# Kernel optimization log

Measured on AMD Instinct MI355X. Metric: run time of the kernel, lower is better.

Reference implementation:

```python
import jax, jax.numpy as jnp
import numpy as np

LN_EPS = 1e-5
NRM_EPS = 1e-12


def layernorm(x, w, b):
    mu = x.mean(-1, keepdims=True)
    var = ((x - mu) ** 2).mean(-1, keepdims=True)
    return (x - mu) * jax.lax.rsqrt(var + LN_EPS) * w + b


def cdist(x, y):
    # Euclidean pairwise distance over trailing (N, C): (..., N, C) x (..., M, C) -> (..., N, M)
    x2 = (x * x).sum(-1)
    y2 = (y * y).sum(-1)
    xy = jnp.einsum('...ic,...jc->...ij', x, y)
    return jnp.sqrt(jnp.maximum(x2[..., :, None] + y2[..., None, :] - 2.0 * xy, NRM_EPS))


def l2norm_last(x):
    n = jnp.sqrt((x * x).sum(-1, keepdims=True))
    return x / jnp.maximum(n, NRM_EPS)


def attn_qcs_sd(anchor, positive, neg1, neg2, k, alpha):
    # anchor/positive: (B,N,C); neg1/neg2: (2,B,N,C)
    # torch.tensor(neg) in the original detaches neg1/neg2 from autograd
    neg1 = jax.lax.stop_gradient(neg1)
    neg2 = jax.lax.stop_gradient(neg2)
    k = k + 1.0
    S_p = cdist(positive, anchor)           # (B,N,N)
    S_p = S_p - S_p.min()
    S_p = S_p.max() - S_p
    S_a = l2norm_last(S_p).sum(1)           # (B,N)
    S_p1 = l2norm_last(jnp.swapaxes(S_p, 1, 2)).sum(1)  # (B,N)

    def proc(D):  # (B,N,N) -> (B,N)
        D = D - D.min()
        return l2norm_last(D).sum(1)

    def pair(neg, tgt):  # neg (2,B,N,C), tgt (B,N,C)
        D = cdist(neg, jnp.broadcast_to(tgt[None], neg.shape))  # (2,B,N,N)
        return proc(D[0]), proc(D[1])

    d11, d12 = pair(neg1, anchor)
    d21, d22 = pair(neg2, anchor)
    map1 = S_a + k * ((d11 + d12) / 2 * alpha + (1 - alpha) * ((d21 + d22) / 2))
    d11, d12 = pair(neg1, positive)
    d21, d22 = pair(neg2, positive)
    map2 = S_p1 + k * ((d11 + d12) / 2 * alpha + (1 - alpha) * ((d21 + d22) / 2))
    return map1[..., None], map2[..., None]  # (B,N,1) each


def setup_inputs() -> dict:
    key = jax.random.key(0)
    B, N, C = 8, 1024, 768
    ks = jax.random.split(key, 12)
    s = 1.0 / np.sqrt(C)
    sh = 1.0 / np.sqrt(4 * C)
    return {
        'anchor': jax.random.normal(ks[0], (B, N, C), jnp.float32),
        'positive': jax.random.normal(ks[1], (B, N, C), jnp.float32),
        'neg1': jax.random.normal(ks[2], (2, B, N, C), jnp.float32),
        'neg2': jax.random.normal(ks[3], (2, B, N, C), jnp.float32),
        'norm1_w': jnp.ones((C,), jnp.float32),
        'norm1_b': jnp.zeros((C,), jnp.float32),
        'norm2_w': jnp.ones((C,), jnp.float32),
        'norm2_b': jnp.zeros((C,), jnp.float32),
        'proj_W': jax.random.uniform(ks[4], (C, 2 * C), jnp.float32, -s, s),
        'proj_b': jax.random.uniform(ks[5], (2 * C,), jnp.float32, -s, s),
        'fc1_W': jax.random.uniform(ks[6], (C, 4 * C), jnp.float32, -s, s),
        'fc1_b': jax.random.uniform(ks[7], (4 * C,), jnp.float32, -s, s),
        'fc2_W': jax.random.uniform(ks[8], (4 * C, C), jnp.float32, -sh, sh),
        'fc2_b': jax.random.uniform(ks[9], (C,), jnp.float32, -sh, sh),
        'theta': jnp.float32(0.0),
        'alpha': jnp.float32(0.0),
    }


def reference(anchor, positive, neg1, neg2, norm1_w, norm1_b, norm2_w, norm2_b,
              proj_W, proj_b, fc1_W, fc1_b, fc2_W, fc2_b, theta, alpha):
    def projsplit(x):
        y = x @ proj_W + proj_b
        C = x.shape[-1]
        return y[..., :C], y[..., C:]  # qk, v

    anc = layernorm(anchor, norm1_w, norm1_b)
    pos = layernorm(positive, norm1_w, norm1_b)
    n1 = layernorm(neg1, norm1_w, norm1_b)   # (2,B,N,C)
    n2 = layernorm(neg2, norm1_w, norm1_b)
    qk_x, v_x = projsplit(anc)
    qk_p, v_p = projsplit(pos)
    qk_n1, v_n1 = projsplit(n1)
    qk_n2, v_n2 = projsplit(n2)

    k = jnp.tanh(theta)
    al = jax.nn.sigmoid(alpha)

    a_a, a_p = attn_qcs_sd(qk_x, qk_p, qk_n1, qk_n2, k, al)
    n1_a, n1_p = attn_qcs_sd(qk_n1[0], qk_n1[1], jnp.stack([qk_x, qk_p]), qk_n2, k, al)
    n2_a, n2_p = attn_qcs_sd(qk_n2[0], qk_n2[1], jnp.stack([qk_x, qk_p]), qk_n1, k, al)

    anc_o = a_a * v_x + anc
    pos_o = a_p * v_p + pos
    neg1_o = jnp.stack([n1_a * v_n1[0] * n1[0], n1_p * v_n1[1] * n1[1]])
    neg2_o = jnp.stack([n2_a * v_n2[0] * n2[0], n2_p * v_n2[1] * n2[1]])

    def block(x):
        h = layernorm(x, norm2_w, norm2_b)
        h = jax.nn.gelu(h @ fc1_W + fc1_b, approximate=False) @ fc2_W + fc2_b
        return h + x

    return block(anc_o), block(pos_o), block(neg1_o), block(neg2_o)
```

## Files before the change

### kernel.cpp

```cpp
#include <hip/hip_runtime.h>
#include <hip/hip_bf16.h>


typedef short bshort8 __attribute__((ext_vector_type(8)));
typedef unsigned short u16x8 __attribute__((ext_vector_type(8)));
typedef float f32x4  __attribute__((ext_vector_type(4)));

#define AS1 __attribute__((address_space(1)))
#define AS3 __attribute__((address_space(3)))

#define B_   8
#define N_   1024
#define C_   768
#define MT   8192
#define M6   49152

#define OFF_QKNORM   0ull
#define OFF_MAPS     196608ull
#define OFF_STATS    393216ull
#define OFF_WBUF     2359296ull
#define OFF_MM       3342336ull
#define MEMSET_BYTES 3342464ull
#define OFF_WTPROJ   3342592ull
#define OFF_WTFC1    5701888ull
#define OFF_WTFC2    10420480ull
#define OFF_LNBF     15139072ull
#define OFF_QKBF     90636544ull
#define OFF_XHBF     OFF_QKBF
#define OFF_VBF      166134016ull
#define OFF_DBUF     241631488ull
#define OFF_H1BF     OFF_DBUF

__constant__ int cSU[15] = {1,3,5, 2,3,4,5, 2,3,4,5, 4,5,4,5};
__constant__ int cSV[15] = {0,2,4, 0,0,0,0, 1,1,1,1, 2,2,3,3};
__constant__ int cTA[15] = {0,0,0, 1,1,2,2, 1,1,2,2, 2,2,2,2};
__constant__ int cTB[15] = {0,0,0, 1,1,1,1, 1,1,1,1, 2,2,2,2};

__device__ __forceinline__ void gll16(const void* g, void* l) {
    __builtin_amdgcn_global_load_lds((const AS1 unsigned int*)g,
                                     (AS3 unsigned int*)l, 16, 0, 0);
}
__device__ __forceinline__ unsigned short f2bu(float v) {
    __hip_bfloat16 h = __float2bfloat16(v);
    return *reinterpret_cast<unsigned short*>(&h);
}
__device__ __forceinline__ float bu2f(unsigned short u) {
    __hip_bfloat16 h;
    *reinterpret_cast<unsigned short*>(&h) = u;
    return __bfloat162float(h);
}
__device__ __forceinline__ int xcd_swz(int flat, int nwg) {
    return (flat & 7) * (nwg >> 3) + (flat >> 3);
}

__device__ __forceinline__ void gemm_core(const __hip_bfloat16* __restrict__ A,
                                          const __hip_bfloat16* __restrict__ Bt,
                                          int lda, int ldb, int kIters,
                                          char* smem, f32x4 acc[4][4])
{
    const int tid  = threadIdx.x;
    const int w    = tid >> 6;
    const int L    = tid & 63;
    const int srow = L >> 2;
    const int schunk = (L & 3) ^ ((L >> 3) & 3);

    const char* ga0 = (const char*)(A  + (size_t)(32*w      + srow) * lda + schunk*8);
    const char* ga1 = (const char*)(A  + (size_t)(32*w + 16 + srow) * lda + schunk*8);
    const char* gb0 = (const char*)(Bt + (size_t)(32*w      + srow) * ldb + schunk*8);
    const char* gb1 = (const char*)(Bt + (size_t)(32*w + 16 + srow) * ldb + schunk*8);
    const int la0 = (32*w)*64;
    const int la1 = (32*w+16)*64;
    const int lb0 = 8192 + (32*w)*64;
    const int lb1 = 8192 + (32*w+16)*64;

    const int m = L & 15, q = L >> 4;
    const int wr = (w >> 1) * 64, wc = (w & 1) * 64;
    const int roff = 16 * (q ^ ((m >> 1) & 3));
    int ra[4], rb[4];
#pragma unroll
    for (int s = 0; s < 4; ++s) {
        ra[s] = (wr + 16*s + m) * 64 + roff;
        rb[s] = 8192 + (wc + 16*s + m) * 64 + roff;
    }
    f32x4 z = {0.f, 0.f, 0.f, 0.f};
#pragma unroll
    for (int s = 0; s < 4; ++s)
#pragma unroll
        for (int t = 0; t < 4; ++t) acc[s][t] = z;

    char* b0 = smem;
    char* b1 = smem + 16384;

    gll16(ga0, b0 + la0); gll16(ga1, b0 + la1);
    gll16(gb0, b0 + lb0); gll16(gb1, b0 + lb1);
    ga0 += 64; ga1 += 64; gb0 += 64; gb1 += 64;

    auto step = [&](char* cur, char* nxt, bool last) {
        __syncthreads();
        if (!last) {
            gll16(ga0, nxt + la0); gll16(ga1, nxt + la1);
            gll16(gb0, nxt + lb0); gll16(gb1, nxt + lb1);
            ga0 += 64; ga1 += 64; gb0 += 64; gb1 += 64;
        }
        bshort8 af[4], bfr[4];
#pragma unroll
        for (int s = 0; s < 4; ++s) af[s]  = *(const bshort8*)(cur + ra[s]);
#pragma unroll
        for (int t = 0; t < 4; ++t) bfr[t] = *(const bshort8*)(cur + rb[t]);
#pragma unroll
        for (int s = 0; s < 4; ++s)
#pragma unroll
            for (int t = 0; t < 4; ++t)
                acc[s][t] = __builtin_amdgcn_mfma_f32_16x16x32_bf16(af[s], bfr[t], acc[s][t], 0, 0, 0);
    };

    for (int kt = 0; kt < kIters; kt += 2) {
        step(b0, b1, false);
        step(b1, b0, kt + 2 >= kIters);
    }
}

__global__ __launch_bounds__(256) void transpose_conv(const float* __restrict__ in,
                                                      __hip_bfloat16* __restrict__ out,
                                                      int R, int C)
{
    __shared__ float tile[32][33];
    int bx = blockIdx.x * 32, by = blockIdx.y * 32;
    int tx = threadIdx.x, ty = threadIdx.y;
#pragma unroll
    for (int i = 0; i < 32; i += 8)
        tile[ty + i][tx] = in[(size_t)(by + ty + i) * C + bx + tx];
    __syncthreads();
#pragma unroll
    for (int i = 0; i < 32; i += 8)
        out[(size_t)(bx + ty + i) * R + by + tx] = __float2bfloat16(tile[tx][ty + i]);
}

__global__ void init_mm(unsigned int* mm)
{
    int i = threadIdx.x;
    if (i < 15) { mm[i] = 0x7f800000u; mm[15 + i] = 0u; }
}

__global__ __launch_bounds__(256) void ln1_kernel(const float* __restrict__ anchor,
                                                  const float* __restrict__ positive,
                                                  const float* __restrict__ neg1,
                                                  const float* __restrict__ neg2,
                                                  const float* __restrict__ w1,
                                                  const float* __restrict__ b1,
                                                  __hip_bfloat16* __restrict__ lnbf)
{
    int w = threadIdx.x >> 6, L = threadIdx.x & 63;
    int r = blockIdx.x * 4 + w;
    int t = r >> 13, within = r & 8191;
    const float* src;
    if      (t == 0) src = anchor   + (size_t)within * C_;
    else if (t == 1) src = positive + (size_t)within * C_;
    else if (t <  4) src = neg1 + ((size_t)(t - 2) * MT + within) * C_;
    else             src = neg2 + ((size_t)(t - 4) * MT + within) * C_;
    float4 x[3]; float s = 0.f, sq = 0.f;
#pragma unroll
    for (int j = 0; j < 3; ++j) {
        x[j] = *(const float4*)(src + 4 * L + 256 * j);
        s  += x[j].x + x[j].y + x[j].z + x[j].w;
        sq += x[j].x*x[j].x + x[j].y*x[j].y + x[j].z*x[j].z + x[j].w*x[j].w;
    }
#pragma unroll
    for (int o = 1; o < 64; o <<= 1) { s += __shfl_xor(s, o, 64); sq += __shfl_xor(sq, o, 64); }
    float mu  = s * (1.f / 768.f);
    float var = sq * (1.f / 768.f) - mu * mu;
    float rs  = rsqrtf(var + 1e-5f);
    __hip_bfloat16* dst = lnbf + (size_t)r * C_;
#pragma unroll
    for (int j = 0; j < 3; ++j) {
        int c = 4 * L + 256 * j;
        float4 wv = *(const float4*)(w1 + c);
        float4 bv = *(const float4*)(b1 + c);
        ushort4 o;
        o.x = f2bu((x[j].x - mu) * rs * wv.x + bv.x);
        o.y = f2bu((x[j].y - mu) * rs * wv.y + bv.y);
        o.z = f2bu((x[j].z - mu) * rs * wv.z + bv.z);
        o.w = f2bu((x[j].w - mu) * rs * wv.w + bv.w);
        *(ushort4*)(dst + c) = o;
    }
}

__global__ __launch_bounds__(256) void gemm_proj(const __hip_bfloat16* __restrict__ A,
                                                 const __hip_bfloat16* __restrict__ Wt,
                                                 const float* __restrict__ bias,
                                                 __hip_bfloat16* __restrict__ qkbf,
                                                 __hip_bfloat16* __restrict__ vbf,
                                                 float* __restrict__ qknorm)
{
    __shared__ __align__(16) char smem[32768];
    int flat = blockIdx.x + 12 * blockIdx.y;
    int sf   = xcd_swz(flat, 12 * 384);
    int bx = sf % 12, by = sf / 12;
    f32x4 acc[4][4];
    gemm_core(A + (size_t)by * 128 * C_, Wt + (size_t)bx * 128 * C_,
              C_, C_, 24, smem, acc);
    int tid = threadIdx.x, w = tid >> 6, L = tid & 63, m = L & 15, q = L >> 4;
    int rowBase = by * 128 + (w >> 1) * 64;
    int colBase = bx * 128 + (w & 1) * 64;
    bool isQK = (bx < 6);
#pragma unroll
    for (int s = 0; s < 4; ++s) {
#pragma unroll
        for (int r = 0; r < 4; ++r) {
            int row = rowBase + 16 * s + 4 * q + r;
            float sqsum = 0.f;
#pragma unroll
            for (int t = 0; t < 4; ++t) {
                int col = colBase + 16 * t + m;
                float val = acc[s][t][r] + bias[col];
                if (isQK) {
                    qkbf[(size_t)row * C_ + col] = __float2bfloat16(val);
                    sqsum += val * val;
                } else {
                    vbf[(size_t)row * C_ + (col - C_)] = __float2bfloat16(val);
                }
            }
            if (isQK) {
#pragma unroll
                for (int o = 1; o < 16; o <<= 1) sqsum += __shfl_xor(sqsum, o, 64);
                if (m == 0) atomicAdd(qknorm + row, sqsum);
            }
        }
    }
}

__global__ __launch_bounds__(256) void gram_kernel(const __hip_bfloat16* __restrict__ qkbf,
                                                   const float* __restrict__ qknorm,
                                                   __hip_bfloat16* __restrict__ Dbuf,
                                                   float* __restrict__ stats,
                                                   unsigned int* __restrict__ mm,
                                                   int sb)
{
    __shared__ __align__(16) char smem[32768];
    int flat = blockIdx.x + 64 * blockIdx.y + 512 * blockIdx.z;
    int nwg  = 512 * gridDim.z;
    int sf   = xcd_swz(flat, nwg);
    int tile = sf & 63;
    int b    = (sf >> 6) & 7;
    int z    = sf >> 9;
    int slab = sb + z;
    int ti = tile >> 3, tj = tile & 7;
    int u = cSU[slab], v = cSV[slab];

    const __hip_bfloat16* Ab = qkbf + (size_t)(u * MT + b * N_ + ti * 128) * C_;
    const __hip_bfloat16* Bb = qkbf + (size_t)(v * MT + b * N_ + tj * 128) * C_;
    f32x4 acc[4][4];
    gemm_core(Ab, Bb, C_, C_, 24, smem, acc);

    int tid = threadIdx.x, w = tid >> 6, L = tid & 63, m = L & 15, q = L >> 4;
    int rowBase = ti * 128 + (w >> 1) * 64;
    int colBase = tj * 128 + (w & 1) * 64;
    const float* nu = qknorm + u * MT + b * N_;
    const float* nv = qknorm + v * MT + b * N_;
    float nbv[4];
#pragma unroll
    for (int t = 0; t < 4; ++t) nbv[t] = nv[colBase + 16 * t + m];

    unsigned short* Dc = (unsigned short*)Dbuf + (size_t)z * 8388608ull
                         + ((size_t)b << 20) + (size_t)tile * 16384 + w * 4096;
    float* rs1 = stats + (size_t)slab * 32768;
    float* rs2 = rs1 + 8192;
    float* cs1 = rs1 + 16384;
    float* cs2 = rs1 + 24576;

    float dmin = 3.0e38f, dmax = 0.f;
    float col1[4] = {0.f,0.f,0.f,0.f}, col2[4] = {0.f,0.f,0.f,0.f};
#pragma unroll
    for (int s = 0; s < 4; ++s) {
        float na[4];
#pragma unroll
        for (int r = 0; r < 4; ++r) na[r] = nu[rowBase + 16 * s + 4 * q + r];
        float dv[4][4];
        float h1v[4] = {0.f,0.f,0.f,0.f}, h2v[4] = {0.f,0.f,0.f,0.f};
#pragma unroll
        for (int t = 0; t < 4; ++t) {
#pragma unroll
            for (int r = 0; r < 4; ++r) {
                float d = sqrtf(fmaxf(na[r] + nbv[t] - 2.f * acc[s][t][r], 1e-12f));
                dv[t][r] = d;
                h1v[r] += d; h2v[r] += d * d;
                col1[t] += d; col2[t] += d * d;
                dmin = fminf(dmin, d); dmax = fmaxf(dmax, d);
            }
        }
#pragma unroll
        for (int tp = 0; tp < 2; ++tp) {
            u16x8 pk;
#pragma unroll
            for (int e = 0; e < 8; ++e)
                pk[e] = f2bu(dv[2 * tp + (e >> 2)][e & 3]);
            *(u16x8*)(Dc + (s * 2 + tp) * 512 + m * 32 + q * 8) = pk;
        }
#pragma unroll
        for (int r = 0; r < 4; ++r) {
            float h1 = h1v[r], h2 = h2v[r];
#pragma unroll
            for (int o = 1; o < 16; o <<= 1) { h1 += __shfl_xor(h1, o, 64); h2 += __shfl_xor(h2, o, 64); }
            if (m == 0) {
                int row = rowBase + 16 * s + 4 * q + r;
                atomicAdd(rs1 + b * N_ + row, h1);
                atomicAdd(rs2 + b * N_ + row, h2);
            }
        }
    }
#pragma unroll
    for (int t = 0; t < 4; ++t) {
        float c1 = col1[t], c2 = col2[t];
        c1 += __shfl_xor(c1, 16, 64); c1 += __shfl_xor(c1, 32, 64);
        c2 += __shfl_xor(c2, 16, 64); c2 += __shfl_xor(c2, 32, 64);
        if (q == 0) {
            int col = colBase + 16 * t + m;
            atomicAdd(cs1 + b * N_ + col, c1);
            atomicAdd(cs2 + b * N_ + col, c2);
        }
    }
#pragma unroll
    for (int o = 1; o < 64; o <<= 1) {
        dmin = fminf(dmin, __shfl_xor(dmin, o, 64));
        dmax = fmaxf(dmax, __shfl_xor(dmax, o, 64));
    }
    if (L == 0) {
        atomicMin(mm + slab, __float_as_uint(dmin));
        atomicMax(mm + 15 + slab, __float_as_uint(dmax));
    }
}

__global__ __launch_bounds__(256) void weights_kernel(const float* __restrict__ stats,
                                                      const unsigned int* __restrict__ mm,
                                                      float* __restrict__ wbuf,
                                                      float* __restrict__ maps,
                                                      const float* __restrict__ theta,
                                                      const float* __restrict__ alpha,
                                                      int sb)
{
    int job = blockIdx.x, b = blockIdx.y;
    int slab = sb + (job >> 1);
    int useB = job & 1;
    const float* s1 = stats + (size_t)slab * 32768 + useB * 16384;
    const float* s2 = s1 + 8192;
    int type = useB ? cTB[slab] : cTA[slab];
    int dst  = useB ? cSU[slab] : cSV[slab];
    float off = (type == 0) ? __uint_as_float(mm[15 + slab]) : __uint_as_float(mm[slab]);
    float k  = tanhf(theta[0]) + 1.0f;
    float al = 1.0f / (1.0f + expf(-alpha[0]));
    float cf = (type == 0) ? -1.0f : ((type == 1) ? 0.5f * k * al : 0.5f * k * (1.0f - al));
    float* wout = wbuf + (size_t)slab * 16384 + useB * 8192 + b * N_;

    float sumw = 0.f;
    for (int i = threadIdx.x; i < N_; i += 256) {
        float a1 = s1[b * N_ + i], a2 = s2[b * N_ + i];
        float nrm2  = fmaxf(a2 - 2.f * off * a1 + (float)N_ * off * off, 0.f);
        float denom = fmaxf(sqrtf(nrm2), 1e-12f);
        float wv = cf / denom;
        wout[i] = wv;
        sumw += wv;
    }
    int w = threadIdx.x >> 6, L = threadIdx.x & 63;
#pragma unroll
    for (int o = 1; o < 64; o <<= 1) sumw += __shfl_xor(sumw, o, 64);
    __shared__ float red[4];
    if (L == 0) red[w] = sumw;
    __syncthreads();
    float tot = red[0] + red[1] + red[2] + red[3];
    float Cb = -off * tot;
    for (int j = threadIdx.x; j < N_; j += 256)
        atomicAdd(maps + (size_t)dst * MT + b * N_ + j, Cb);
}

__global__ __launch_bounds__(256) void wsum_kernel(const __hip_bfloat16* __restrict__ Dbuf,
                                                   const float* __restrict__ wbuf,
                                                   float* __restrict__ maps,
                                                   int sb)
{
    int z = blockIdx.z, slab = sb + z, b = blockIdx.y;
    int tile = blockIdx.x;
    int ti = tile >> 3, tj = tile & 7;
    int u = cSU[slab], v = cSV[slab];
    int tid = threadIdx.x, w = tid >> 6, L = tid & 63, m = L & 15, q = L >> 4;
    const unsigned short* Dc = (const unsigned short*)Dbuf + (size_t)z * 8388608ull
                               + ((size_t)b << 20) + (size_t)tile * 16384 + w * 4096;
    const float* wr = wbuf + (size_t)slab * 16384 + b * N_ + ti * 128;
    const float* wc = wbuf + (size_t)slab * 16384 + 8192 + b * N_ + tj * 128;

    __shared__ float swr[128], swc[128];
    if (threadIdx.x < 128) swr[threadIdx.x] = wr[threadIdx.x];
    else                   swc[threadIdx.x - 128] = wc[threadIdx.x - 128];
    __syncthreads();

    int wrbase = (w >> 1) * 64, wcbase = (w & 1) * 64;
    float wc1[4];
#pragma unroll
    for (int t = 0; t < 4; ++t) wc1[t] = swc[wcbase + 16 * t + m];
    float wr4[4][4];
#pragma unroll
    for (int s = 0; s < 4; ++s)
#pragma unroll
        for (int r = 0; r < 4; ++r) wr4[s][r] = swr[wrbase + 16 * s + 4 * q + r];

    float rowacc[4][4];
#pragma unroll
    for (int s = 0; s < 4; ++s)
#pragma unroll
        for (int r = 0; r < 4; ++r) rowacc[s][r] = 0.f;
    float colacc[4] = {0.f,0.f,0.f,0.f};

#pragma unroll
    for (int s = 0; s < 4; ++s) {
#pragma unroll
        for (int tp = 0; tp < 2; ++tp) {
            u16x8 d8 = *(const u16x8*)(Dc + (s * 2 + tp) * 512 + m * 32 + q * 8);
#pragma unroll
            for (int e = 0; e < 8; ++e) {
                int t = 2 * tp + (e >> 2), r = e & 3;
                float d = bu2f(d8[e]);
                rowacc[s][r] += wc1[t] * d;
                colacc[t]    += wr4[s][r] * d;
            }
        }
    }
#pragma unroll
    for (int s = 0; s < 4; ++s)
#pragma unroll
        for (int r = 0; r < 4; ++r) {
            float h = rowacc[s][r];
#pragma unroll
            for (int o = 1; o < 16; o <<= 1) h += __shfl_xor(h, o, 64);
            if (m == 0)
                atomicAdd(maps + (size_t)u * MT + b * N_ + ti * 128 + wrbase + 16 * s + 4 * q + r, h);
        }
#pragma unroll
    for (int t = 0; t < 4; ++t) {
        float c = colacc[t];
        c += __shfl_xor(c, 16, 64); c += __shfl_xor(c, 32, 64);
        if (q == 0)
            atomicAdd(maps + (size_t)v * MT + b * N_ + tj * 128 + wcbase + 16 * t + m, c);
    }
}

__global__ __launch_bounds__(256) void combine_ln2(const float* __restrict__ maps,
                                                   const __hip_bfloat16* __restrict__ vbf,
                                                   const __hip_bfloat16* __restrict__ lnbf,
                                                   const float* __restrict__ w2,
                                                   const float* __restrict__ b2,
                                                   float* __restrict__ dout,
                                                   __hip_bfloat16* __restrict__ xhbf)
{
    int w = threadIdx.x >> 6, L = threadIdx.x & 63;
    int r = blockIdx.x * 4 + w;
    int t = r >> 13;
    float mv = maps[r];
    const __hip_bfloat16* vp = vbf + (size_t)r * C_;
    const __hip_bfloat16* lp = lnbf + (size_t)r * C_;
    float x[12]; float s = 0.f, sq = 0.f;
#pragma unroll
    for (int j = 0; j < 3; ++j) {
        int c = 4 * L + 256 * j;
        ushort4 vv = *(const ushort4*)(vp + c);
        ushort4 ll = *(const ushort4*)(lp + c);
        float xv[4];
        xv[0] = (t < 2) ? (mv * bu2f(vv.x) + bu2f(ll.x)) : (mv * bu2f(vv.x) * bu2f(ll.x));
        xv[1] = (t < 2) ? (mv * bu2f(vv.y) + bu2f(ll.y)) : (mv * bu2f(vv.y) * bu2f(ll.y));
        xv[2] = (t < 2) ? (mv * bu2f(vv.z) + bu2f(ll.z)) : (mv * bu2f(vv.z) * bu2f(ll.z));
        xv[3] = (t < 2) ? (mv * bu2f(vv.w) + bu2f(ll.w)) : (mv * bu2f(vv.w) * bu2f(ll.w));
        float4 xo = {xv[0], xv[1], xv[2], xv[3]};
        *(float4*)(dout + (size_t)r * C_ + c) = xo;
#pragma unroll
        for (int e = 0; e < 4; ++e) { x[4*j+e] = xv[e]; s += xv[e]; sq += xv[e]*xv[e]; }
    }
#pragma unroll
    for (int o = 1; o < 64; o <<= 1) { s += __shfl_xor(s, o, 64); sq += __shfl_xor(sq, o, 64); }
    float mu  = s * (1.f / 768.f);
    float var = sq * (1.f / 768.f) - mu * mu;
    float rs  = rsqrtf(var + 1e-5f);
    __hip_bfloat16* dst = xhbf + (size_t)r * C_;
#pragma unroll
    for (int j = 0; j < 3; ++j) {
        int c = 4 * L + 256 * j;
        float4 wv = *(const float4*)(w2 + c);
        float4 bv = *(const float4*)(b2 + c);
        ushort4 o;
        o.x = f2bu((x[4*j+0] - mu) * rs * wv.x + bv.x);
        o.y = f2bu((x[4*j+1] - mu) * rs * wv.y + bv.y);
        o.z = f2bu((x[4*j+2] - mu) * rs * wv.z + bv.z);
        o.w = f2bu((x[4*j+3] - mu) * rs * wv.w + bv.w);
        *(ushort4*)(dst + c) = o;
    }
}

__global__ __launch_bounds__(256) void gemm_ffn1(const __hip_bfloat16* __restrict__ A,
                                                 const __hip_bfloat16* __restrict__ Wt,
                                                 const float* __restrict__ bias,
                                                 __hip_bfloat16* __restrict__ h1)
{
    __shared__ __align__(16) char smem[32768];
    int flat = blockIdx.x + 24 * blockIdx.y;
    int sf   = xcd_swz(flat, 24 * 192);
    int bx = sf % 24, by = sf / 24;
    f32x4 acc[4][4];
    gemm_core(A + (size_t)by * 128 * C_, Wt + (size_t)bx * 128 * C_,
              C_, C_, 24, smem, acc);
    int tid = threadIdx.x, w = tid >> 6, L = tid & 63, m = L & 15, q = L >> 4;
    int rowBase = by * 128 + (w >> 1) * 64;
    int colBase = bx * 128 + (w & 1) * 64;
#pragma unroll
    for (int s = 0; s < 4; ++s)
#pragma unroll
        for (int r = 0; r < 4; ++r) {
            int row = rowBase + 16 * s + 4 * q + r;
#pragma unroll
            for (int t = 0; t < 4; ++t) {
                int col = colBase + 16 * t + m;
                float val = acc[s][t][r] + bias[col];
                float ge  = 0.5f * val * (1.0f + erff(val * 0.70710678118654752f));
                h1[(size_t)row * 3072 + col] = __float2bfloat16(ge);
            }
        }
}

__global__ __launch_bounds__(256) void gemm_ffn2(const __hip_bfloat16* __restrict__ A,
                                                 const __hip_bfloat16* __restrict__ Wt,
                                                 const float* __restrict__ bias,
                                                 float* __restrict__ out)
{
    __shared__ __align__(16) char smem[32768];
    int flat = blockIdx.x + 6 * blockIdx.y;
    int sf   = xcd_swz(flat, 6 * 192);
    int bx = sf % 6, by = sf / 6;
    f32x4 acc[4][4];
    gemm_core(A + (size_t)by * 128 * 3072, Wt + (size_t)bx * 128 * 3072,
              3072, 3072, 96, smem, acc);
    int tid = threadIdx.x, w = tid >> 6, L = tid & 63, m = L & 15, q = L >> 4;
    int rowBase = by * 128 + (w >> 1) * 64;
    int colBase = bx * 128 + (w & 1) * 64;
#pragma unroll
    for (int s = 0; s < 4; ++s)
#pragma unroll
        for (int r = 0; r < 4; ++r) {
            int row = rowBase + 16 * s + 4 * q + r;
#pragma unroll
            for (int t = 0; t < 4; ++t) {
                int col = colBase + 16 * t + m;
                size_t idx = (size_t)row * C_ + col;
                out[idx] = out[idx] + acc[s][t][r] + bias[col];
            }
        }
}

extern "C" void kernel_launch(void* const* d_in, const int* in_sizes, int n_in,
                              void* d_out, int out_size, void* d_ws, size_t ws_size,
                              hipStream_t stream)
{
    (void)in_sizes; (void)n_in; (void)out_size; (void)ws_size;
    const float* anchor   = (const float*)d_in[0];
    const float* positive = (const float*)d_in[1];
    const float* neg1     = (const float*)d_in[2];
    const float* neg2     = (const float*)d_in[3];
    const float* n1w      = (const float*)d_in[4];
    const float* n1b      = (const float*)d_in[5];
    const float* n2w      = (const float*)d_in[6];
    const float* n2b      = (const float*)d_in[7];
    const float* projW    = (const float*)d_in[8];
    const float* projb    = (const float*)d_in[9];
    const float* fc1W     = (const float*)d_in[10];
    const float* fc1b     = (const float*)d_in[11];
    const float* fc2W     = (const float*)d_in[12];
    const float* fc2b     = (const float*)d_in[13];
    const float* theta    = (const float*)d_in[14];
    const float* alpha    = (const float*)d_in[15];
    float* dout = (float*)d_out;

    char* ws = (char*)d_ws;
    float*          qknorm = (float*)(ws + OFF_QKNORM);
    float*          maps   = (float*)(ws + OFF_MAPS);
    float*          stats  = (float*)(ws + OFF_STATS);
    float*          wbuf   = (float*)(ws + OFF_WBUF);
    unsigned int*   mm     = (unsigned int*)(ws + OFF_MM);
    __hip_bfloat16* WtProj = (__hip_bfloat16*)(ws + OFF_WTPROJ);
    __hip_bfloat16* WtFc1  = (__hip_bfloat16*)(ws + OFF_WTFC1);
    __hip_bfloat16* WtFc2  = (__hip_bfloat16*)(ws + OFF_WTFC2);
    __hip_bfloat16* lnbf   = (__hip_bfloat16*)(ws + OFF_LNBF);
    __hip_bfloat16* qkbf   = (__hip_bfloat16*)(ws + OFF_QKBF);
    __hip_bfloat16* xhbf   = (__hip_bfloat16*)(ws + OFF_XHBF);
    __hip_bfloat16* vbf    = (__hip_bfloat16*)(ws + OFF_VBF);
    __hip_bfloat16* Dbuf   = (__hip_bfloat16*)(ws + OFF_DBUF);
    __hip_bfloat16* h1bf   = (__hip_bfloat16*)(ws + OFF_H1BF);

    hipMemsetAsync(ws, 0, MEMSET_BYTES, stream);
    init_mm<<<1, 64, 0, stream>>>(mm);

    transpose_conv<<<dim3(48, 24), dim3(32, 8), 0, stream>>>(projW, WtProj, 768, 1536);
    transpose_conv<<<dim3(96, 24), dim3(32, 8), 0, stream>>>(fc1W,  WtFc1,  768, 3072);
    transpose_conv<<<dim3(24, 96), dim3(32, 8), 0, stream>>>(fc2W,  WtFc2,  3072, 768);

    ln1_kernel<<<12288, 256, 0, stream>>>(anchor, positive, neg1, neg2, n1w, n1b, lnbf);

    gemm_proj<<<dim3(12, 384), 256, 0, stream>>>(lnbf, WtProj, projb, qkbf, vbf, qknorm);

    for (int g = 0; g < 2; ++g) {
        int sb = g * 8;
        int ns = g ? 7 : 8;
        gram_kernel<<<dim3(64, 8, ns), 256, 0, stream>>>(qkbf, qknorm, Dbuf, stats, mm, sb);
        weights_kernel<<<dim3(2 * ns, 8), 256, 0, stream>>>(stats, mm, wbuf, maps, theta, alpha, sb);
        wsum_kernel<<<dim3(64, 8, ns), 256, 0, stream>>>(Dbuf, wbuf, maps, sb);
    }

    combine_ln2<<<12288, 256, 0, stream>>>(maps, vbf, lnbf, n2w, n2b, dout, xhbf);

    for (int ch = 0; ch < 2; ++ch) {
        size_t ro = (size_t)ch * 24576;
        gemm_ffn1<<<dim3(24, 192), 256, 0, stream>>>(xhbf + ro * C_, WtFc1, fc1b, h1bf);
        gemm_ffn2<<<dim3(6, 192), 256, 0, stream>>>(h1bf, WtFc2, fc2b, dout + ro * C_);
    }
}
```

Before: 1.971 ms.

## Enlarge GEMM block tiles to 256x256 with 512-thread workgroups

Replaces the 128x128 shared GEMM core with a 256x256 tile computed by 8 waves, each wave owning a 128x64 sub-tile. The K step grows to 64 and LDS becomes a 128 KB double buffer with an XOR swizzle. Projection, Gram-distance and both FFN GEMMs move to the new core, with grids and epilogue indexing remapped and bias loads hoisted out of the epilogue loops. The aim is more operand reuse per LDS and global load. In exchange, each workgroup uses far more LDS and registers, so occupancy likely drops and there are fewer workgroups to spread over the CUs.

```diff
diff --git a/kernel.cpp b/kernel.cpp
--- a/kernel.cpp
+++ b/kernel.cpp
@@ -53,70 +53,70 @@
     return (flat & 7) * (nwg >> 3) + (flat >> 3);
 }
 
-__device__ __forceinline__ void gemm_core(const __hip_bfloat16* __restrict__ A,
-                                          const __hip_bfloat16* __restrict__ Bt,
-                                          int lda, int ldb, int kIters,
-                                          char* smem, f32x4 acc[4][4])
-{
-    const int tid  = threadIdx.x;
-    const int w    = tid >> 6;
-    const int L    = tid & 63;
-    const int srow = L >> 2;
-    const int schunk = (L & 3) ^ ((L >> 3) & 3);
-
-    const char* ga0 = (const char*)(A  + (size_t)(32*w      + srow) * lda + schunk*8);
-    const char* ga1 = (const char*)(A  + (size_t)(32*w + 16 + srow) * lda + schunk*8);
-    const char* gb0 = (const char*)(Bt + (size_t)(32*w      + srow) * ldb + schunk*8);
-    const char* gb1 = (const char*)(Bt + (size_t)(32*w + 16 + srow) * ldb + schunk*8);
-    const int la0 = (32*w)*64;
-    const int la1 = (32*w+16)*64;
-    const int lb0 = 8192 + (32*w)*64;
-    const int lb1 = 8192 + (32*w+16)*64;
-
-    const int m = L & 15, q = L >> 4;
-    const int wr = (w >> 1) * 64, wc = (w & 1) * 64;
-    const int roff = 16 * (q ^ ((m >> 1) & 3));
-    int ra[4], rb[4];
-#pragma unroll
-    for (int s = 0; s < 4; ++s) {
-        ra[s] = (wr + 16*s + m) * 64 + roff;
-        rb[s] = 8192 + (wc + 16*s + m) * 64 + roff;
-    }
+__device__ __forceinline__ void gemm256_core(const __hip_bfloat16* __restrict__ A,
+                                             const __hip_bfloat16* __restrict__ Bt,
+                                             int lda, int ldb, int kTiles,
+                                             char* smem, f32x4 acc[8][4])
+{
+    const int tid = threadIdx.x;
+    const int L   = tid & 63;
+    const int m   = L & 15, q = L >> 4;
+    const int w   = tid >> 6;
+    const int wm  = w >> 2, wn = w & 3;
+
+    const char* gA[4]; const char* gB[4];
+    int lA[4], lB[4];
+#pragma unroll
+    for (int i = 0; i < 4; ++i) {
+        int c  = tid + 512 * i;
+        int r  = c >> 3;
+        int gk = (c & 7) ^ (r & 7);
+        gA[i] = (const char*)(A  + (size_t)r * lda) + gk * 16;
+        gB[i] = (const char*)(Bt + (size_t)r * ldb) + gk * 16;
+        lA[i] = c * 16;
+        lB[i] = 32768 + c * 16;
+    }
+    const int aBase = wm * 16384 + m * 128;
+    const int bBase = 32768 + wn * 8192 + m * 128;
+    const int s0    = (q ^ (m & 7)) * 16;
+
     f32x4 z = {0.f, 0.f, 0.f, 0.f};
 #pragma unroll
-    for (int s = 0; s < 4; ++s)
-#pragma unroll
-        for (int t = 0; t < 4; ++t) acc[s][t] = z;
-
-    char* b0 = smem;
-    char* b1 = smem + 16384;
-
-    gll16(ga0, b0 + la0); gll16(ga1, b0 + la1);
-    gll16(gb0, b0 + lb0); gll16(gb1, b0 + lb1);
-    ga0 += 64; ga1 += 64; gb0 += 64; gb1 += 64;
-
-    auto step = [&](char* cur, char* nxt, bool last) {
+    for (int i = 0; i < 8; ++i)
+#pragma unroll
+        for (int j = 0; j < 4; ++j) acc[i][j] = z;
+
+#pragma unroll
+    for (int i = 0; i < 4; ++i) { gll16(gA[i], smem + lA[i]); gll16(gB[i], smem + lB[i]); }
+
+    for (int kt = 0; kt < kTiles; ++kt) {
         __syncthreads();
-        if (!last) {
-            gll16(ga0, nxt + la0); gll16(ga1, nxt + la1);
-            gll16(gb0, nxt + lb0); gll16(gb1, nxt + lb1);
-            ga0 += 64; ga1 += 64; gb0 += 64; gb1 += 64;
-        }
-        bshort8 af[4], bfr[4];
-#pragma unroll
-        for (int s = 0; s < 4; ++s) af[s]  = *(const bshort8*)(cur + ra[s]);
-#pragma unroll
-        for (int t = 0; t < 4; ++t) bfr[t] = *(const bshort8*)(cur + rb[t]);
-#pragma unroll
-        for (int s = 0; s < 4; ++s)
-#pragma unroll
-            for (int t = 0; t < 4; ++t)
-                acc[s][t] = __builtin_amdgcn_mfma_f32_16x16x32_bf16(af[s], bfr[t], acc[s][t], 0, 0, 0);
-    };
-
-    for (int kt = 0; kt < kIters; kt += 2) {
-        step(b0, b1, false);
-        step(b1, b0, kt + 2 >= kIters);
+        char* cur = smem + (kt & 1) * 65536;
+        if (kt + 1 < kTiles) {
+            char* nxt = smem + ((kt + 1) & 1) * 65536;
+            const int adv = (kt + 1) * 128;
+#pragma unroll
+            for (int i = 0; i < 4; ++i) {
+                gll16(gA[i] + adv, nxt + lA[i]);
+                gll16(gB[i] + adv, nxt + lB[i]);
+            }
+        }
+#pragma unroll
+        for (int ks = 0; ks < 2; ++ks) {
+            const int so = s0 ^ (ks * 64);
+            bshort8 af[8], bf[4];
+#pragma unroll
+            for (int mi = 0; mi < 8; ++mi)
+                af[mi] = *(const bshort8*)(cur + aBase + mi * 2048 + so);
+#pragma unroll
+            for (int nj = 0; nj < 4; ++nj)
+                bf[nj] = *(const bshort8*)(cur + bBase + nj * 2048 + so);
+#pragma unroll
+            for (int mi = 0; mi < 8; ++mi)
+#pragma unroll
+                for (int nj = 0; nj < 4; ++nj)
+                    acc[mi][nj] = __builtin_amdgcn_mfma_f32_16x16x32_bf16(af[mi], bf[nj], acc[mi][nj], 0, 0, 0);
+        }
     }
 }
 
@@ -185,34 +185,38 @@
     }
 }
 
-__global__ __launch_bounds__(256) void gemm_proj(const __hip_bfloat16* __restrict__ A,
-                                                 const __hip_bfloat16* __restrict__ Wt,
-                                                 const float* __restrict__ bias,
-                                                 __hip_bfloat16* __restrict__ qkbf,
-                                                 __hip_bfloat16* __restrict__ vbf,
-                                                 float* __restrict__ qknorm)
-{
-    __shared__ __align__(16) char smem[32768];
-    int flat = blockIdx.x + 12 * blockIdx.y;
-    int sf   = xcd_swz(flat, 12 * 384);
-    int bx = sf % 12, by = sf / 12;
-    f32x4 acc[4][4];
-    gemm_core(A + (size_t)by * 128 * C_, Wt + (size_t)bx * 128 * C_,
-              C_, C_, 24, smem, acc);
+__global__ __launch_bounds__(512, 2) void gemm_proj(const __hip_bfloat16* __restrict__ A,
+                                                    const __hip_bfloat16* __restrict__ Wt,
+                                                    const float* __restrict__ bias,
+                                                    __hip_bfloat16* __restrict__ qkbf,
+                                                    __hip_bfloat16* __restrict__ vbf,
+                                                    float* __restrict__ qknorm)
+{
+    __shared__ __align__(16) char smem[131072];
+    int flat = blockIdx.x + 6 * blockIdx.y;
+    int sf   = xcd_swz(flat, 6 * 192);
+    int bx = sf % 6, by = sf / 6;
+    f32x4 acc[8][4];
+    gemm256_core(A + (size_t)by * 256 * C_, Wt + (size_t)bx * 256 * C_,
+                 C_, C_, 12, smem, acc);
     int tid = threadIdx.x, w = tid >> 6, L = tid & 63, m = L & 15, q = L >> 4;
-    int rowBase = by * 128 + (w >> 1) * 64;
-    int colBase = bx * 128 + (w & 1) * 64;
-    bool isQK = (bx < 6);
-#pragma unroll
-    for (int s = 0; s < 4; ++s) {
+    int wm = w >> 2, wn = w & 3;
+    int rowBase = by * 256 + wm * 128;
+    int colBase = bx * 256 + wn * 64;
+    bool isQK = (bx < 3);
+    float bv[4];
+#pragma unroll
+    for (int nj = 0; nj < 4; ++nj) bv[nj] = bias[colBase + nj * 16 + m];
+#pragma unroll
+    for (int mi = 0; mi < 8; ++mi) {
 #pragma unroll
         for (int r = 0; r < 4; ++r) {
-            int row = rowBase + 16 * s + 4 * q + r;
+            int row = rowBase + mi * 16 + 4 * q + r;
             float sqsum = 0.f;
 #pragma unroll
-            for (int t = 0; t < 4; ++t) {
-                int col = colBase + 16 * t + m;
-                float val = acc[s][t][r] + bias[col];
+            for (int nj = 0; nj < 4; ++nj) {
+                int col = colBase + nj * 16 + m;
+                float val = acc[mi][nj][r] + bv[nj];
                 if (isQK) {
                     qkbf[(size_t)row * C_ + col] = __float2bfloat16(val);
                     sqsum += val * val;
@@ -229,40 +233,41 @@
     }
 }
 
-__global__ __launch_bounds__(256) void gram_kernel(const __hip_bfloat16* __restrict__ qkbf,
-                                                   const float* __restrict__ qknorm,
-                                                   __hip_bfloat16* __restrict__ Dbuf,
-                                                   float* __restrict__ stats,
-                                                   unsigned int* __restrict__ mm,
-                                                   int sb)
-{
-    __shared__ __align__(16) char smem[32768];
-    int flat = blockIdx.x + 64 * blockIdx.y + 512 * blockIdx.z;
-    int nwg  = 512 * gridDim.z;
+__global__ __launch_bounds__(512, 2) void gram_kernel(const __hip_bfloat16* __restrict__ qkbf,
+                                                      const float* __restrict__ qknorm,
+                                                      __hip_bfloat16* __restrict__ Dbuf,
+                                                      float* __restrict__ stats,
+                                                      unsigned int* __restrict__ mm,
+                                                      int sb)
+{
+    __shared__ __align__(16) char smem[131072];
+    int flat = blockIdx.x + 16 * blockIdx.y + 128 * blockIdx.z;
+    int nwg  = 128 * gridDim.z;
     int sf   = xcd_swz(flat, nwg);
-    int tile = sf & 63;
-    int b    = (sf >> 6) & 7;
-    int z    = sf >> 9;
+    int tile = sf & 15;
+    int b    = (sf >> 4) & 7;
+    int z    = sf >> 7;
     int slab = sb + z;
-    int ti = tile >> 3, tj = tile & 7;
+    int TI = tile >> 2, TJ = tile & 3;
     int u = cSU[slab], v = cSV[slab];
 
-    const __hip_bfloat16* Ab = qkbf + (size_t)(u * MT + b * N_ + ti * 128) * C_;
-    const __hip_bfloat16* Bb = qkbf + (size_t)(v * MT + b * N_ + tj * 128) * C_;
-    f32x4 acc[4][4];
-    gemm_core(Ab, Bb, C_, C_, 24, smem, acc);
+    const __hip_bfloat16* Ab = qkbf + (size_t)(u * MT + b * N_ + TI * 256) * C_;
+    const __hip_bfloat16* Bb = qkbf + (size_t)(v * MT + b * N_ + TJ * 256) * C_;
+    f32x4 acc[8][4];
+    gemm256_core(Ab, Bb, C_, C_, 12, smem, acc);
 
     int tid = threadIdx.x, w = tid >> 6, L = tid & 63, m = L & 15, q = L >> 4;
-    int rowBase = ti * 128 + (w >> 1) * 64;
-    int colBase = tj * 128 + (w & 1) * 64;
+    int wm = w >> 2, wn = w & 3;
+    int rowBase = TI * 256 + wm * 128;
+    int colBase = TJ * 256 + wn * 64;
     const float* nu = qknorm + u * MT + b * N_;
     const float* nv = qknorm + v * MT + b * N_;
     float nbv[4];
 #pragma unroll
-    for (int t = 0; t < 4; ++t) nbv[t] = nv[colBase + 16 * t + m];
-
-    unsigned short* Dc = (unsigned short*)Dbuf + (size_t)z * 8388608ull
-                         + ((size_t)b << 20) + (size_t)tile * 16384 + w * 4096;
+    for (int nj = 0; nj < 4; ++nj) nbv[nj] = nv[colBase + nj * 16 + m];
+
+    unsigned short* Dz = (unsigned short*)Dbuf + (size_t)z * 8388608ull + ((size_t)b << 20);
+    int tile128 = (TI * 2 + wm) * 8 + TJ * 2 + (wn >> 1);
     float* rs1 = stats + (size_t)slab * 32768;
     float* rs2 = rs1 + 8192;
     float* cs1 = rs1 + 16384;
@@ -271,30 +276,33 @@
     float dmin = 3.0e38f, dmax = 0.f;
     float col1[4] = {0.f,0.f,0.f,0.f}, col2[4] = {0.f,0.f,0.f,0.f};
 #pragma unroll
-    for (int s = 0; s < 4; ++s) {
+    for (int mi = 0; mi < 8; ++mi) {
         float na[4];
 #pragma unroll
-        for (int r = 0; r < 4; ++r) na[r] = nu[rowBase + 16 * s + 4 * q + r];
+        for (int r = 0; r < 4; ++r) na[r] = nu[rowBase + mi * 16 + 4 * q + r];
         float dv[4][4];
         float h1v[4] = {0.f,0.f,0.f,0.f}, h2v[4] = {0.f,0.f,0.f,0.f};
 #pragma unroll
-        for (int t = 0; t < 4; ++t) {
+        for (int nj = 0; nj < 4; ++nj) {
 #pragma unroll
             for (int r = 0; r < 4; ++r) {
-                float d = sqrtf(fmaxf(na[r] + nbv[t] - 2.f * acc[s][t][r], 1e-12f));
-                dv[t][r] = d;
+                float d = sqrtf(fmaxf(na[r] + nbv[nj] - 2.f * acc[mi][nj][r], 1e-12f));
+                dv[nj][r] = d;
                 h1v[r] += d; h2v[r] += d * d;
-                col1[t] += d; col2[t] += d * d;
+                col1[nj] += d; col2[nj] += d * d;
                 dmin = fminf(dmin, d); dmax = fmaxf(dmax, d);
             }
         }
+        unsigned short* base = Dz + (size_t)tile128 * 16384
+                             + (((mi >> 2) << 1) | (wn & 1)) * 4096
+                             + ((mi & 3) * 2) * 512 + m * 32 + q * 8;
 #pragma unroll
         for (int tp = 0; tp < 2; ++tp) {
             u16x8 pk;
 #pragma unroll
             for (int e = 0; e < 8; ++e)
                 pk[e] = f2bu(dv[2 * tp + (e >> 2)][e & 3]);
-            *(u16x8*)(Dc + (s * 2 + tp) * 512 + m * 32 + q * 8) = pk;
+            *(u16x8*)(base + tp * 512) = pk;
         }
 #pragma unroll
         for (int r = 0; r < 4; ++r) {
@@ -302,19 +310,19 @@
 #pragma unroll
             for (int o = 1; o < 16; o <<= 1) { h1 += __shfl_xor(h1, o, 64); h2 += __shfl_xor(h2, o, 64); }
             if (m == 0) {
-                int row = rowBase + 16 * s + 4 * q + r;
+                int row = rowBase + mi * 16 + 4 * q + r;
                 atomicAdd(rs1 + b * N_ + row, h1);
                 atomicAdd(rs2 + b * N_ + row, h2);
             }
         }
     }
 #pragma unroll
-    for (int t = 0; t < 4; ++t) {
-        float c1 = col1[t], c2 = col2[t];
+    for (int nj = 0; nj < 4; ++nj) {
+        float c1 = col1[nj], c2 = col2[nj];
         c1 += __shfl_xor(c1, 16, 64); c1 += __shfl_xor(c1, 32, 64);
         c2 += __shfl_xor(c2, 16, 64); c2 += __shfl_xor(c2, 32, 64);
         if (q == 0) {
-            int col = colBase + 16 * t + m;
+            int col = colBase + nj * 16 + m;
             atomicAdd(cs1 + b * N_ + col, c1);
             atomicAdd(cs2 + b * N_ + col, c2);
         }
@@ -492,61 +500,69 @@
     }
 }
 
-__global__ __launch_bounds__(256) void gemm_ffn1(const __hip_bfloat16* __restrict__ A,
-                                                 const __hip_bfloat16* __restrict__ Wt,
-                                                 const float* __restrict__ bias,
-                                                 __hip_bfloat16* __restrict__ h1)
-{
-    __shared__ __align__(16) char smem[32768];
-    int flat = blockIdx.x + 24 * blockIdx.y;
-    int sf   = xcd_swz(flat, 24 * 192);
-    int bx = sf % 24, by = sf / 24;
-    f32x4 acc[4][4];
-    gemm_core(A + (size_t)by * 128 * C_, Wt + (size_t)bx * 128 * C_,
-              C_, C_, 24, smem, acc);
+__global__ __launch_bounds__(512, 2) void gemm_ffn1(const __hip_bfloat16* __restrict__ A,
+                                                    const __hip_bfloat16* __restrict__ Wt,
+                                                    const float* __restrict__ bias,
+                                                    __hip_bfloat16* __restrict__ h1)
+{
+    __shared__ __align__(16) char smem[131072];
+    int flat = blockIdx.x + 12 * blockIdx.y;
+    int sf   = xcd_swz(flat, 12 * 96);
+    int bx = sf % 12, by = sf / 12;
+    f32x4 acc[8][4];
+    gemm256_core(A + (size_t)by * 256 * C_, Wt + (size_t)bx * 256 * C_,
+                 C_, C_, 12, smem, acc);
     int tid = threadIdx.x, w = tid >> 6, L = tid & 63, m = L & 15, q = L >> 4;
-    int rowBase = by * 128 + (w >> 1) * 64;
-    int colBase = bx * 128 + (w & 1) * 64;
-#pragma unroll
-    for (int s = 0; s < 4; ++s)
+    int wm = w >> 2, wn = w & 3;
+    int rowBase = by * 256 + wm * 128;
+    int colBase = bx * 256 + wn * 64;
+    float bv[4];
+#pragma unroll
+    for (int nj = 0; nj < 4; ++nj) bv[nj] = bias[colBase + nj * 16 + m];
+#pragma unroll
+    for (int mi = 0; mi < 8; ++mi)
 #pragma unroll
         for (int r = 0; r < 4; ++r) {
-            int row = rowBase + 16 * s + 4 * q + r;
-#pragma unroll
-            for (int t = 0; t < 4; ++t) {
-                int col = colBase + 16 * t + m;
-                float val = acc[s][t][r] + bias[col];
+            int row = rowBase + mi * 16 + 4 * q + r;
+#pragma unroll
+            for (int nj = 0; nj < 4; ++nj) {
+                int col = colBase + nj * 16 + m;
+                float val = acc[mi][nj][r] + bv[nj];
                 float ge  = 0.5f * val * (1.0f + erff(val * 0.70710678118654752f));
                 h1[(size_t)row * 3072 + col] = __float2bfloat16(ge);
             }
         }
 }
 
-__global__ __launch_bounds__(256) void gemm_ffn2(const __hip_bfloat16* __restrict__ A,
-                                                 const __hip_bfloat16* __restrict__ Wt,
-                                                 const float* __restrict__ bias,
-                                                 float* __restrict__ out)
-{
-    __shared__ __align__(16) char smem[32768];
-    int flat = blockIdx.x + 6 * blockIdx.y;
-    int sf   = xcd_swz(flat, 6 * 192);
-    int bx = sf % 6, by = sf / 6;
-    f32x4 acc[4][4];
-    gemm_core(A + (size_t)by * 128 * 3072, Wt + (size_t)bx * 128 * 3072,
-              3072, 3072, 96, smem, acc);
+__global__ __launch_bounds__(512, 2) void gemm_ffn2(const __hip_bfloat16* __restrict__ A,
+                                                    const __hip_bfloat16* __restrict__ Wt,
+                                                    const float* __restrict__ bias,
+                                                    float* __restrict__ out)
+{
+    __shared__ __align__(16) char smem[131072];
+    int flat = blockIdx.x + 3 * blockIdx.y;
+    int sf   = xcd_swz(flat, 3 * 96);
+    int bx = sf % 3, by = sf / 3;
+    f32x4 acc[8][4];
+    gemm256_core(A + (size_t)by * 256 * 3072, Wt + (size_t)bx * 256 * 3072,
+                 3072, 3072, 48, smem, acc);
     int tid = threadIdx.x, w = tid >> 6, L = tid & 63, m = L & 15, q = L >> 4;
-    int rowBase = by * 128 + (w >> 1) * 64;
-    int colBase = bx * 128 + (w & 1) * 64;
-#pragma unroll
-    for (int s = 0; s < 4; ++s)
+    int wm = w >> 2, wn = w & 3;
+    int rowBase = by * 256 + wm * 128;
+    int colBase = bx * 256 + wn * 64;
+    float bv[4];
+#pragma unroll
+    for (int nj = 0; nj < 4; ++nj) bv[nj] = bias[colBase + nj * 16 + m];
+#pragma unroll
+    for (int mi = 0; mi < 8; ++mi)
 #pragma unroll
         for (int r = 0; r < 4; ++r) {
-            int row = rowBase + 16 * s + 4 * q + r;
-#pragma unroll
-            for (int t = 0; t < 4; ++t) {
-                int col = colBase + 16 * t + m;
+            int row = rowBase + mi * 16 + 4 * q + r;
+#pragma unroll
+            for (int nj = 0; nj < 4; ++nj) {
+                int col = colBase + nj * 16 + m;
                 size_t idx = (size_t)row * C_ + col;
-                out[idx] = out[idx] + acc[s][t][r] + bias[col];
+                out[idx] = out[idx] + acc[mi][nj][r] + bv[nj];
             }
         }
 }
@@ -599,12 +615,12 @@
 
     ln1_kernel<<<12288, 256, 0, stream>>>(anchor, positive, neg1, neg2, n1w, n1b, lnbf);
 
-    gemm_proj<<<dim3(12, 384), 256, 0, stream>>>(lnbf, WtProj, projb, qkbf, vbf, qknorm);
+    gemm_proj<<<dim3(6, 192), 512, 0, stream>>>(lnbf, WtProj, projb, qkbf, vbf, qknorm);
 
     for (int g = 0; g < 2; ++g) {
         int sb = g * 8;
         int ns = g ? 7 : 8;
-        gram_kernel<<<dim3(64, 8, ns), 256, 0, stream>>>(qkbf, qknorm, Dbuf, stats, mm, sb);
+        gram_kernel<<<dim3(16, 8, ns), 512, 0, stream>>>(qkbf, qknorm, Dbuf, stats, mm, sb);
         weights_kernel<<<dim3(2 * ns, 8), 256, 0, stream>>>(stats, mm, wbuf, maps, theta, alpha, sb);
         wsum_kernel<<<dim3(64, 8, ns), 256, 0, stream>>>(Dbuf, wbuf, maps, sb);
     }
@@ -613,7 +629,7 @@
 
     for (int ch = 0; ch < 2; ++ch) {
         size_t ro = (size_t)ch * 24576;
-        gemm_ffn1<<<dim3(24, 192), 256, 0, stream>>>(xhbf + ro * C_, WtFc1, fc1b, h1bf);
-        gemm_ffn2<<<dim3(6, 192), 256, 0, stream>>>(h1bf, WtFc2, fc2b, dout + ro * C_);
-    }
-}
+        gemm_ffn1<<<dim3(12, 96), 512, 0, stream>>>(xhbf + ro * C_, WtFc1, fc1b, h1bf);
+        gemm_ffn2<<<dim3(3, 96), 512, 0, stream>>>(h1bf, WtFc2, fc2b, dout + ro * C_);
+    }
+}
```

Measured after the change: 1.720 ms. 12.8% less time.
